# Kernel tuning notes

Hardware: AMD Instinct MI355X
Metric: run time of the kernel (lower is better)

Reference implementation:

```python
import jax, jax.numpy as jnp
import numpy as np

B, L, D, I, E, K = 2, 2048, 1024, 4096, 8, 2
LN_EPS = 1e-5


def _layernorm(x, g, b):
    m = jnp.mean(x, axis=-1, keepdims=True)
    v = jnp.mean(jnp.square(x - m), axis=-1, keepdims=True)
    return (x - m) * jax.lax.rsqrt(v + LN_EPS) * g + b


def setup_inputs() -> dict:
    key = jax.random.key(0)
    ks = jax.random.split(key, 4)
    return {
        "hidden_states": jax.random.normal(ks[0], (B, L, D), dtype=jnp.float32),
        "rn_g": jnp.ones((D,), jnp.float32),
        "rn_b": jnp.zeros((D,), jnp.float32),
        "router_w": jax.random.normal(ks[1], (E, D), jnp.float32) * 0.02,
        "router_b": jnp.zeros((E,), jnp.float32),
        "ln_g": jnp.ones((E, D), jnp.float32),
        "ln_b": jnp.zeros((E, D), jnp.float32),
        "w1": jax.random.normal(ks[2], (E, D, I), jnp.float32) * 0.02,
        "b1": jnp.zeros((E, I), jnp.float32),
        "w2": jax.random.normal(ks[3], (E, I, D), jnp.float32) * 0.02,
        "b2": jnp.zeros((E, D), jnp.float32),
    }


def reference(hidden_states, rn_g, rn_b, router_w, router_b, ln_g, ln_b, w1, b1, w2, b2):
    # Router (dropout is identity in eval mode)
    normed = _layernorm(hidden_states, rn_g, rn_b)
    logits = (jnp.einsum('bld,ed->ble', normed, router_w) + router_b).astype(jnp.float32)
    top_w, top_idx = jax.lax.top_k(logits, K)                    # [B,L,K]
    top_w = jax.nn.softmax(top_w, axis=-1).astype(hidden_states.dtype)
    # Per-token combine weight for each expert: sum over selected slots
    onehot = jax.nn.one_hot(top_idx, E, dtype=top_w.dtype)       # [B,L,K,E]
    combine = jnp.einsum('blke,blk->ble', onehot, top_w)         # [B,L,E]

    out = jnp.zeros_like(hidden_states)
    for e in range(E):  # fixed, small expert count
        h = _layernorm(hidden_states, ln_g[e], ln_b[e])
        h = jax.nn.gelu(jnp.einsum('bld,di->bli', h, w1[e]) + b1[e], approximate=False)
        h = jnp.einsum('bli,id->bld', h, w2[e]) + b2[e]
        out = out + combine[..., e:e + 1] * h
    return out
```

## Files before the change

kernel.cpp:

```cpp
#include <hip/hip_runtime.h>
#include <hip/hip_bf16.h>
#include <stdint.h>

#define T_TOK 4096
#define DDIM  1024
#define IDIM  4096
#define NEXP  8
#define GROWS (T_TOK*2 + 128)

typedef __attribute__((ext_vector_type(8))) short bfrag;
typedef __attribute__((ext_vector_type(4))) float f32x4;

__device__ __forceinline__ unsigned short f2bf(float x) {
    unsigned int u = __float_as_uint(x);
    unsigned int r = u + 0x7FFFu + ((u >> 16) & 1u);
    return (unsigned short)(r >> 16);
}
__device__ __forceinline__ float bf2f(unsigned short h) {
    return __uint_as_float(((unsigned int)h) << 16);
}

__global__ __launch_bounds__(256) void router_kernel(
    const float* __restrict__ x,
    const float* __restrict__ rng, const float* __restrict__ rnb,
    const float* __restrict__ rw,  const float* __restrict__ rb,
    unsigned short* __restrict__ xhat,
    int* __restrict__ counts, int* __restrict__ tok_slot,
    float* __restrict__ wslot)
{
    const int t = blockIdx.x;
    const int tid = threadIdx.x;
    const int lane = tid & 63, wid = tid >> 6;

    float4 v = *(const float4*)(x + (size_t)t * DDIM + tid * 4);
    float s1 = v.x + v.y + v.z + v.w;
    float s2 = v.x*v.x + v.y*v.y + v.z*v.z + v.w*v.w;
    #pragma unroll
    for (int m = 32; m; m >>= 1) { s1 += __shfl_xor(s1, m, 64); s2 += __shfl_xor(s2, m, 64); }

    __shared__ float red[8];
    __shared__ float pl[4][8];
    __shared__ float bcast[2];
    if (lane == 0) { red[wid] = s1; red[wid + 4] = s2; }
    __syncthreads();
    if (tid == 0) {
        float S1 = red[0] + red[1] + red[2] + red[3];
        float S2 = red[4] + red[5] + red[6] + red[7];
        float mean = S1 * (1.f / 1024.f);
        float var  = S2 * (1.f / 1024.f) - mean * mean;
        bcast[0] = mean; bcast[1] = rsqrtf(var + 1e-5f);
    }
    __syncthreads();
    const float mean = bcast[0], rinv = bcast[1];

    float4 xh = { (v.x - mean) * rinv, (v.y - mean) * rinv,
                  (v.z - mean) * rinv, (v.w - mean) * rinv };
    ushort4 hx = { f2bf(xh.x), f2bf(xh.y), f2bf(xh.z), f2bf(xh.w) };
    *(ushort4*)(xhat + (size_t)t * DDIM + tid * 4) = hx;

    float4 g = *(const float4*)(rng + tid * 4);
    float4 b = *(const float4*)(rnb + tid * 4);
    float4 nm = { xh.x*g.x + b.x, xh.y*g.y + b.y, xh.z*g.z + b.z, xh.w*g.w + b.w };
    float p[8];
    #pragma unroll
    for (int e = 0; e < 8; e++) {
        float4 w = *(const float4*)(rw + e * DDIM + tid * 4);
        p[e] = nm.x*w.x + nm.y*w.y + nm.z*w.z + nm.w*w.w;
    }
    #pragma unroll
    for (int m = 32; m; m >>= 1) {
        #pragma unroll
        for (int e = 0; e < 8; e++) p[e] += __shfl_xor(p[e], m, 64);
    }
    if (lane == 0) {
        #pragma unroll
        for (int e = 0; e < 8; e++) pl[wid][e] = p[e];
    }
    __syncthreads();
    if (tid == 0) {
        float l[8];
        #pragma unroll
        for (int e = 0; e < 8; e++) l[e] = pl[0][e] + pl[1][e] + pl[2][e] + pl[3][e] + rb[e];
        int e0 = 0; float v0 = l[0];
        for (int e = 1; e < 8; e++) if (l[e] > v0) { v0 = l[e]; e0 = e; }
        int e1 = (e0 == 0) ? 1 : 0; float v1 = l[e1];
        for (int e = 0; e < 8; e++) if (e != e0 && l[e] > v1) { v1 = l[e]; e1 = e; }
        float ex = expf(v1 - v0);
        float w0 = 1.f / (1.f + ex);
        float w1 = ex * w0;
        int p0 = atomicAdd(&counts[e0], 1);
        tok_slot[e0 * T_TOK + p0] = (t << 1);
        int p1 = atomicAdd(&counts[e1], 1);
        tok_slot[e1 * T_TOK + p1] = (t << 1) | 1;
        wslot[t * 2]     = w0;
        wslot[t * 2 + 1] = w1;
    }
}

__global__ void prefix_kernel(const int* __restrict__ counts, int* __restrict__ offs)
{
    if (threadIdx.x == 0) {
        int a = 0;
        for (int e = 0; e < 8; e++) { offs[e] = a; a += counts[e]; }
    }
}

__global__ __launch_bounds__(256) void gather_kernel(
    const unsigned short* __restrict__ xhat,
    const float* __restrict__ lng, const float* __restrict__ lnb,
    const int* __restrict__ counts, const int* __restrict__ offs,
    const int* __restrict__ tok_slot,
    unsigned short* __restrict__ Agath, int* __restrict__ rowinfo)
{
    const int e = blockIdx.y, pos = blockIdx.x;
    if (pos >= counts[e]) return;
    const int grow = offs[e] + pos;
    const int info = tok_slot[e * T_TOK + pos];
    if (threadIdx.x == 0) rowinfo[grow] = info;
    const int t = info >> 1;
    const int d = threadIdx.x * 4;
    ushort4 hx = *(const ushort4*)(xhat + (size_t)t * DDIM + d);
    float4 g = *(const float4*)(lng + (size_t)e * DDIM + d);
    float4 b = *(const float4*)(lnb + (size_t)e * DDIM + d);
    ushort4 o = { f2bf(bf2f(hx.x) * g.x + b.x),
                  f2bf(bf2f(hx.y) * g.y + b.y),
                  f2bf(bf2f(hx.z) * g.z + b.z),
                  f2bf(bf2f(hx.w) * g.w + b.w) };
    *(ushort4*)(Agath + (size_t)grow * DDIM + d) = o;
}

template<int EPI>
__global__ __launch_bounds__(256) void gemm_kernel(
    const unsigned short* __restrict__ Asrc,
    const float* __restrict__ Wsrc,
    const float* __restrict__ bias,
    const int* __restrict__ counts,
    const int* __restrict__ offs,
    const int* __restrict__ rowinfo,
    const float* __restrict__ wslot,
    unsigned short* __restrict__ Hout,
    float* __restrict__ Out,
    int Kd, int Nd)
{
    const int e  = blockIdx.z;
    const int ne = counts[e];
    const int mt = blockIdx.y;
    if (mt * 128 >= ne) return;
    const int n0 = blockIdx.x * 128;
    const int growbase = offs[e] + mt * 128;
    const int tid  = threadIdx.x;
    const int lane = tid & 63;
    const int wm = (tid >> 7) & 1;
    const int wn = (tid >> 6) & 1;

    __shared__ unsigned short As[128 * 72];
    __shared__ unsigned short Bs[128 * 72];

    f32x4 acc[4][4];
    #pragma unroll
    for (int i = 0; i < 4; i++)
        #pragma unroll
        for (int j = 0; j < 4; j++)
            acc[i][j] = (f32x4){0.f, 0.f, 0.f, 0.f};

    const float* W = Wsrc + (size_t)e * Kd * Nd;

    for (int k0 = 0; k0 < Kd; k0 += 64) {
        __syncthreads();
        #pragma unroll
        for (int c = 0; c < 4; c++) {
            int ci = c * 256 + tid;
            int row = ci >> 3, s = ci & 7;
            int4 v = *(const int4*)(Asrc + (size_t)(growbase + row) * Kd + k0 + s * 8);
            *(int4*)((char*)As + row * 144 + s * 16) = v;
        }
        #pragma unroll
        for (int q = 0; q < 2; q++) {
            int bi = q * 256 + tid;
            int nb = bi & 63;
            int kb = bi >> 6;
            int n  = nb * 2;
            const float* wp = W + (size_t)(k0 + kb * 8) * Nd + n0 + n;
            float2 f[8];
            #pragma unroll
            for (int r = 0; r < 8; r++) f[r] = *(const float2*)(wp + (size_t)r * Nd);
            int4 va, vb;
            va.x = (int)(((unsigned)f2bf(f[0].x)) | ((unsigned)f2bf(f[1].x) << 16));
            va.y = (int)(((unsigned)f2bf(f[2].x)) | ((unsigned)f2bf(f[3].x) << 16));
            va.z = (int)(((unsigned)f2bf(f[4].x)) | ((unsigned)f2bf(f[5].x) << 16));
            va.w = (int)(((unsigned)f2bf(f[6].x)) | ((unsigned)f2bf(f[7].x) << 16));
            vb.x = (int)(((unsigned)f2bf(f[0].y)) | ((unsigned)f2bf(f[1].y) << 16));
            vb.y = (int)(((unsigned)f2bf(f[2].y)) | ((unsigned)f2bf(f[3].y) << 16));
            vb.z = (int)(((unsigned)f2bf(f[4].y)) | ((unsigned)f2bf(f[5].y) << 16));
            vb.w = (int)(((unsigned)f2bf(f[6].y)) | ((unsigned)f2bf(f[7].y) << 16));
            *(int4*)((char*)Bs + (size_t)n       * 144 + kb * 16) = va;
            *(int4*)((char*)Bs + (size_t)(n + 1) * 144 + kb * 16) = vb;
        }
        __syncthreads();
        #pragma unroll
        for (int kk = 0; kk < 2; kk++) {
            bfrag av[4], bv[4];
            #pragma unroll
            for (int i = 0; i < 4; i++)
                av[i] = *(const bfrag*)((const char*)As +
                         (wm * 64 + i * 16 + (lane & 15)) * 144 + kk * 64 + ((lane >> 4) << 4));
            #pragma unroll
            for (int j = 0; j < 4; j++)
                bv[j] = *(const bfrag*)((const char*)Bs +
                         (wn * 64 + j * 16 + (lane & 15)) * 144 + kk * 64 + ((lane >> 4) << 4));
            #pragma unroll
            for (int i = 0; i < 4; i++)
                #pragma unroll
                for (int j = 0; j < 4; j++)
                    acc[i][j] = __builtin_amdgcn_mfma_f32_16x16x32_bf16(av[i], bv[j], acc[i][j], 0, 0, 0);
        }
    }

    const float* bg = bias + (size_t)e * Nd;
    #pragma unroll
    for (int i = 0; i < 4; i++) {
        #pragma unroll
        for (int r = 0; r < 4; r++) {
            int mrow = wm * 64 + i * 16 + ((lane >> 4) << 2) + r;
            int pos = mt * 128 + mrow;
            if (pos >= ne) continue;
            if constexpr (EPI == 0) {
                size_t rowoff = (size_t)(growbase + mrow) * Nd;
                #pragma unroll
                for (int j = 0; j < 4; j++) {
                    int col = n0 + wn * 64 + j * 16 + (lane & 15);
                    float y = acc[i][j][r] + bg[col];
                    float gl = 0.5f * y * (1.f + erff(y * 0.70710678118654752f));
                    Hout[rowoff + col] = f2bf(gl);
                }
            } else {
                int info = rowinfo[growbase + mrow];
                float wg = wslot[info];
                float* op = Out + (size_t)(info >> 1) * Nd;
                #pragma unroll
                for (int j = 0; j < 4; j++) {
                    int col = n0 + wn * 64 + j * 16 + (lane & 15);
                    float y = acc[i][j][r] + bg[col];
                    atomicAdd(op + col, wg * y);
                }
            }
        }
    }
}

extern "C" void kernel_launch(void* const* d_in, const int* in_sizes, int n_in,
                              void* d_out, int out_size, void* d_ws, size_t ws_size,
                              hipStream_t stream)
{
    (void)in_sizes; (void)n_in; (void)ws_size;
    const float* hidden   = (const float*)d_in[0];
    const float* rn_g     = (const float*)d_in[1];
    const float* rn_b     = (const float*)d_in[2];
    const float* router_w = (const float*)d_in[3];
    const float* router_b = (const float*)d_in[4];
    const float* ln_g     = (const float*)d_in[5];
    const float* ln_b     = (const float*)d_in[6];
    const float* w1       = (const float*)d_in[7];
    const float* b1       = (const float*)d_in[8];
    const float* w2       = (const float*)d_in[9];
    const float* b2       = (const float*)d_in[10];
    float* out = (float*)d_out;

    char* ws = (char*)d_ws;
    unsigned short* xhat   = (unsigned short*)ws;
    unsigned short* Agath  = (unsigned short*)(ws + 8388608);
    unsigned short* H      = (unsigned short*)(ws + 25427968);
    int*   counts   = (int*)(ws + 93585408);
    int*   offs     = (int*)(ws + 93585440);
    int*   tok_slot = (int*)(ws + 93585472);
    int*   rowinfo  = (int*)(ws + 93716544);
    float* wslot    = (float*)(ws + 93749824);

    hipMemsetAsync(counts, 0, 64, stream);
    hipMemsetAsync(d_out, 0, (size_t)out_size * sizeof(float), stream);

    router_kernel<<<T_TOK, 256, 0, stream>>>(hidden, rn_g, rn_b, router_w, router_b,
                                             xhat, counts, tok_slot, wslot);
    prefix_kernel<<<1, 64, 0, stream>>>(counts, offs);
    gather_kernel<<<dim3(T_TOK, NEXP), 256, 0, stream>>>(xhat, ln_g, ln_b, counts, offs,
                                                         tok_slot, Agath, rowinfo);
    gemm_kernel<0><<<dim3(IDIM / 128, 32, NEXP), 256, 0, stream>>>(
        Agath, w1, b1, counts, offs, rowinfo, wslot, H, nullptr, DDIM, IDIM);
    gemm_kernel<1><<<dim3(DDIM / 128, 32, NEXP), 256, 0, stream>>>(
        H, w2, b2, counts, offs, rowinfo, wslot, nullptr, out, IDIM, DDIM);
}
```

Measured before the change: 533.8 us.

## Pre-transpose weights to bf16 and stage GEMM tiles with global_load_lds

Adds a transpose kernel that converts each expert's fp32 weight matrix into a K-contiguous bf16 copy in workspace before each GEMM. The GEMM main loop then loads both A and B tiles straight into LDS with 16-byte global_load_lds instead of per-thread fp32 loads, bf16 conversion and LDS stores, and the LDS padding is removed. This cuts the per-tile conversion work, which was repeated across every M tile, and halves the weight bytes the GEMMs read. In exchange it adds two full passes over the weights, reuses one workspace buffer serially, and unpadded LDS rows may cause bank conflicts on fragment reads.

```diff
diff --git a/kernel.cpp b/kernel.cpp
--- a/kernel.cpp
+++ b/kernel.cpp
@@ -19,6 +19,11 @@
 __device__ __forceinline__ float bf2f(unsigned short h) {
     return __uint_as_float(((unsigned int)h) << 16);
 }
+
+#define GLOAD16(gsrc, ldst)                                                     \
+    __builtin_amdgcn_global_load_lds(                                           \
+        (const __attribute__((address_space(1))) unsigned int*)(gsrc),          \
+        (__attribute__((address_space(3))) unsigned int*)(ldst), 16, 0, 0)
 
 __global__ __launch_bounds__(256) void router_kernel(
     const float* __restrict__ x,
@@ -129,10 +134,28 @@
     *(ushort4*)(Agath + (size_t)grow * DDIM + d) = o;
 }
 
+__global__ __launch_bounds__(256) void transpose_kernel(
+    const float* __restrict__ W, unsigned short* __restrict__ WT,
+    int Kd, int Nd)
+{
+    const int e  = blockIdx.z;
+    const int k0 = blockIdx.y * 64;
+    const int n  = blockIdx.x * 256 + threadIdx.x;
+    const float* src = W + (size_t)e * Kd * Nd + (size_t)k0 * Nd + n;
+    unsigned short* dst = WT + ((size_t)e * Nd + n) * Kd + k0;
+    unsigned short buf[64];
+    #pragma unroll
+    for (int j = 0; j < 64; j++)
+        buf[j] = f2bf(src[(size_t)j * Nd]);
+    #pragma unroll
+    for (int c = 0; c < 8; c++)
+        *(int4*)(dst + c * 8) = *(const int4*)(buf + c * 8);
+}
+
 template<int EPI>
 __global__ __launch_bounds__(256) void gemm_kernel(
     const unsigned short* __restrict__ Asrc,
-    const float* __restrict__ Wsrc,
+    const unsigned short* __restrict__ Bsrc,
     const float* __restrict__ bias,
     const int* __restrict__ counts,
     const int* __restrict__ offs,
@@ -153,8 +176,8 @@
     const int wm = (tid >> 7) & 1;
     const int wn = (tid >> 6) & 1;
 
-    __shared__ unsigned short As[128 * 72];
-    __shared__ unsigned short Bs[128 * 72];
+    __shared__ unsigned short As[128 * 64];
+    __shared__ unsigned short Bs[128 * 64];
 
     f32x4 acc[4][4];
     #pragma unroll
@@ -163,39 +186,20 @@
         for (int j = 0; j < 4; j++)
             acc[i][j] = (f32x4){0.f, 0.f, 0.f, 0.f};
 
-    const float* W = Wsrc + (size_t)e * Kd * Nd;
+    const unsigned short* ap = Asrc + (size_t)(growbase + (tid >> 3)) * Kd + (tid & 7) * 8;
+    const unsigned short* bp = Bsrc + ((size_t)e * Nd + n0 + (tid >> 3)) * Kd + (tid & 7) * 8;
+    char* aldsw = (char*)As + (tid >> 6) * 1024;
+    char* bldsw = (char*)Bs + (tid >> 6) * 1024;
+    const size_t rowstep = (size_t)32 * Kd;
 
     for (int k0 = 0; k0 < Kd; k0 += 64) {
         __syncthreads();
         #pragma unroll
         for (int c = 0; c < 4; c++) {
-            int ci = c * 256 + tid;
-            int row = ci >> 3, s = ci & 7;
-            int4 v = *(const int4*)(Asrc + (size_t)(growbase + row) * Kd + k0 + s * 8);
-            *(int4*)((char*)As + row * 144 + s * 16) = v;
+            GLOAD16(ap + c * rowstep, aldsw + c * 4096);
+            GLOAD16(bp + c * rowstep, bldsw + c * 4096);
         }
-        #pragma unroll
-        for (int q = 0; q < 2; q++) {
-            int bi = q * 256 + tid;
-            int nb = bi & 63;
-            int kb = bi >> 6;
-            int n  = nb * 2;
-            const float* wp = W + (size_t)(k0 + kb * 8) * Nd + n0 + n;
-            float2 f[8];
-            #pragma unroll
-            for (int r = 0; r < 8; r++) f[r] = *(const float2*)(wp + (size_t)r * Nd);
-            int4 va, vb;
-            va.x = (int)(((unsigned)f2bf(f[0].x)) | ((unsigned)f2bf(f[1].x) << 16));
-            va.y = (int)(((unsigned)f2bf(f[2].x)) | ((unsigned)f2bf(f[3].x) << 16));
-            va.z = (int)(((unsigned)f2bf(f[4].x)) | ((unsigned)f2bf(f[5].x) << 16));
-            va.w = (int)(((unsigned)f2bf(f[6].x)) | ((unsigned)f2bf(f[7].x) << 16));
-            vb.x = (int)(((unsigned)f2bf(f[0].y)) | ((unsigned)f2bf(f[1].y) << 16));
-            vb.y = (int)(((unsigned)f2bf(f[2].y)) | ((unsigned)f2bf(f[3].y) << 16));
-            vb.z = (int)(((unsigned)f2bf(f[4].y)) | ((unsigned)f2bf(f[5].y) << 16));
-            vb.w = (int)(((unsigned)f2bf(f[6].y)) | ((unsigned)f2bf(f[7].y) << 16));
-            *(int4*)((char*)Bs + (size_t)n       * 144 + kb * 16) = va;
-            *(int4*)((char*)Bs + (size_t)(n + 1) * 144 + kb * 16) = vb;
-        }
+        ap += 64; bp += 64;
         __syncthreads();
         #pragma unroll
         for (int kk = 0; kk < 2; kk++) {
@@ -203,11 +207,11 @@
             #pragma unroll
             for (int i = 0; i < 4; i++)
                 av[i] = *(const bfrag*)((const char*)As +
-                         (wm * 64 + i * 16 + (lane & 15)) * 144 + kk * 64 + ((lane >> 4) << 4));
+                         (wm * 64 + i * 16 + (lane & 15)) * 128 + kk * 64 + ((lane >> 4) << 4));
             #pragma unroll
             for (int j = 0; j < 4; j++)
                 bv[j] = *(const bfrag*)((const char*)Bs +
-                         (wn * 64 + j * 16 + (lane & 15)) * 144 + kk * 64 + ((lane >> 4) << 4));
+                         (wn * 64 + j * 16 + (lane & 15)) * 128 + kk * 64 + ((lane >> 4) << 4));
             #pragma unroll
             for (int i = 0; i < 4; i++)
                 #pragma unroll
@@ -252,7 +256,7 @@
                               void* d_out, int out_size, void* d_ws, size_t ws_size,
                               hipStream_t stream)
 {
-    (void)in_sizes; (void)n_in; (void)ws_size;
+    (void)in_sizes; (void)n_in;
     const float* hidden   = (const float*)d_in[0];
     const float* rn_g     = (const float*)d_in[1];
     const float* rn_b     = (const float*)d_in[2];
@@ -270,22 +274,26 @@
     unsigned short* xhat   = (unsigned short*)ws;
     unsigned short* Agath  = (unsigned short*)(ws + 8388608);
     unsigned short* H      = (unsigned short*)(ws + 25427968);
-    int*   counts   = (int*)(ws + 93585408);
-    int*   offs     = (int*)(ws + 93585440);
-    int*   tok_slot = (int*)(ws + 93585472);
-    int*   rowinfo  = (int*)(ws + 93716544);
-    float* wslot    = (float*)(ws + 93749824);
+    unsigned short* WT     = (unsigned short*)(ws + 93585408);
+    int*   counts   = (int*)(ws + 160694272);
+    int*   offs     = (int*)(ws + 160694304);
+    int*   tok_slot = (int*)(ws + 160694336);
+    int*   rowinfo  = (int*)(ws + 160825408);
+    float* wslot    = (float*)(ws + 160858688);
+    if (ws_size < 160891456) return;
 
     hipMemsetAsync(counts, 0, 64, stream);
     hipMemsetAsync(d_out, 0, (size_t)out_size * sizeof(float), stream);
 
+    transpose_kernel<<<dim3(IDIM / 256, DDIM / 64, NEXP), 256, 0, stream>>>(w1, WT, DDIM, IDIM);
     router_kernel<<<T_TOK, 256, 0, stream>>>(hidden, rn_g, rn_b, router_w, router_b,
                                              xhat, counts, tok_slot, wslot);
     prefix_kernel<<<1, 64, 0, stream>>>(counts, offs);
     gather_kernel<<<dim3(T_TOK, NEXP), 256, 0, stream>>>(xhat, ln_g, ln_b, counts, offs,
                                                          tok_slot, Agath, rowinfo);
     gemm_kernel<0><<<dim3(IDIM / 128, 32, NEXP), 256, 0, stream>>>(
-        Agath, w1, b1, counts, offs, rowinfo, wslot, H, nullptr, DDIM, IDIM);
+        Agath, WT, b1, counts, offs, rowinfo, wslot, H, nullptr, DDIM, IDIM);
+    transpose_kernel<<<dim3(DDIM / 256, IDIM / 64, NEXP), 256, 0, stream>>>(w2, WT, IDIM, DDIM);
     gemm_kernel<1><<<dim3(DDIM / 128, 32, NEXP), 256, 0, stream>>>(
-        H, w2, b2, counts, offs, rowinfo, wslot, nullptr, out, IDIM, DDIM);
-}
+        H, WT, b2, counts, offs, rowinfo, wslot, nullptr, out, IDIM, DDIM);
+}
```

New measurement: 622.7 us, median of 5. 16.7% more time.
